# Performance work log

Hardware: AMD Instinct MI355X
Metric: run time of the kernel (lower is better)

## Reference

```python
import jax, jax.numpy as jnp
import numpy as np

B, T, V, D, H, L = 4, 2048, 99, 512, 8, 6
DH = D // H
OFFSET = 28  # size_puzzle_tokens = 1 + 26 + 1
GELU_C = 0.7978845608028654  # sqrt(2/pi)
EPS = 1e-5


def layernorm(x, w):
    m = jnp.mean(x, axis=-1, keepdims=True)
    v = jnp.mean(jnp.square(x - m), axis=-1, keepdims=True)
    return (x - m) / jnp.sqrt(v + EPS) * w


def new_gelu(x):
    return 0.5 * x * (1.0 + jnp.tanh(GELU_C * (x + 0.044715 * x ** 3)))


def setup_inputs() -> dict:
    key = jax.random.key(0)
    ks = jax.random.split(key, 12)
    s = 0.02
    return {
        'idx': jax.random.randint(ks[0], (B, T), 0, V),
        'targets': jax.random.randint(ks[1], (B, T), 0, V),
        'wte': jax.random.normal(ks[2], (V, D), jnp.float32) * s,   # tied with lm_head
        'wpe': jax.random.normal(ks[3], (T, D), jnp.float32) * s,
        'ln1_w': jnp.ones((L, D), jnp.float32),
        'attn_w': jax.random.normal(ks[4], (L, 3 * D, D), jnp.float32) * s,
        'proj_w': jax.random.normal(ks[5], (L, D, D), jnp.float32) * (s / np.sqrt(2 * L)),
        'ln2_w': jnp.ones((L, D), jnp.float32),
        'fc_w': jax.random.normal(ks[6], (L, 4 * D, D), jnp.float32) * s,
        'fc_proj_w': jax.random.normal(ks[7], (L, D, 4 * D), jnp.float32) * (s / np.sqrt(2 * L)),
        'lnf_w': jnp.ones((D,), jnp.float32),
    }


def _forward(idx, targets, wte, wpe, ln1_w, attn_w, proj_w, ln2_w, fc_w, fc_proj_w, lnf_w):
    t = idx.shape[1]
    x = wte[idx] + wpe[:t][None]  # [B,T,D]
    # mask: tril(ones(T+28, T)) narrowed from row 28 -> query i attends keys j <= i+28
    q_ids = jnp.arange(t)
    mask = (q_ids[None, :] <= q_ids[:, None] + OFFSET)  # [T,T]
    scale = 1.0 / np.sqrt(DH)

    def block(x, p):
        w1, wa, wp, w2, wf, wfp = p
        h = layernorm(x, w1)
        qkv = jnp.einsum('btc,oc->bto', h, wa)  # [B,T,3D]
        q, k, v = jnp.split(qkv, 3, axis=-1)
        q = q.reshape(B, t, H, DH)
        k = k.reshape(B, t, H, DH)
        v = v.reshape(B, t, H, DH)
        att = jnp.einsum('bqhd,bkhd->bhqk', q, k) * scale
        att = jnp.where(mask[None, None], att, -jnp.inf)
        att = jax.nn.softmax(att, axis=-1)
        y = jnp.einsum('bhqk,bkhd->bqhd', att, v).reshape(B, t, D)
        y = jnp.einsum('btc,oc->bto', y, wp)
        x = x + y
        h2 = layernorm(x, w2)
        m = new_gelu(jnp.einsum('btc,fc->btf', h2, wf))
        x = x + jnp.einsum('btf,cf->btc', m, wfp)
        return x, None

    x, _ = jax.lax.scan(block, x, (ln1_w, attn_w, proj_w, ln2_w, fc_w, fc_proj_w))
    x = layernorm(x, lnf_w)
    logits = jnp.einsum('btd,vd->btv', x, wte)

    # weighted cross entropy, ignore_index=-1
    ce_w = jnp.zeros((V,), jnp.float32).at[78:96].set(1.0).at[96].set(0.1)
    y = targets.reshape(-1)
    valid = (y != -1)
    yc = jnp.where(valid, y, 0)
    logp = jax.nn.log_softmax(logits.reshape(-1, V), axis=-1)
    nll = -jnp.take_along_axis(logp, yc[:, None], axis=1)[:, 0]
    wi = ce_w[yc] * valid.astype(jnp.float32)
    loss = jnp.sum(wi * nll) / jnp.sum(wi)
    return logits, loss


def reference(idx, targets, wte, wpe, ln1_w, attn_w, proj_w, ln2_w, fc_w, fc_proj_w, lnf_w):
    return _forward(idx, targets, wte, wpe, ln1_w, attn_w, proj_w, ln2_w, fc_w, fc_proj_w, lnf_w)
```

## Files before the change

### kernel.cpp

```cpp
#include <hip/hip_runtime.h>
#include <hip/hip_bf16.h>
#include <math.h>

#define BB 4
#define TT 2048
#define VV 99
#define DD 512
#define HH 8
#define LL 6
#define DHH 64
#define OFFS 28
#define ROWS (BB*TT)

typedef __hip_bfloat16 bf16;
typedef __attribute__((ext_vector_type(8))) short bf16x8;
typedef __attribute__((ext_vector_type(4))) short s16x4;
typedef __attribute__((ext_vector_type(4))) float f32x4;

__device__ __forceinline__ float b2f(bf16 x){ return __bfloat162float(x); }

__device__ __forceinline__ void async_copy16(const void* g, void* l){
    __builtin_amdgcn_global_load_lds(
        (const __attribute__((address_space(1))) unsigned int*)g,
        (__attribute__((address_space(3))) unsigned int*)l, 16, 0, 0);
}

__device__ __forceinline__ unsigned lds_off(const void* p){
    return (unsigned)(size_t)(const __attribute__((address_space(3))) char*)p;
}

#define TRD(dst, a, lit) asm volatile("ds_read_b64_tr_b16 %0, %1 offset:" lit \
                                      : "=v"(dst) : "v"(a) : "memory")
#define CAT8(lo, hi) ((bf16x8)__builtin_shufflevector((lo), (hi), 0,1,2,3,4,5,6,7))

__device__ __forceinline__ unsigned pk2(float a, float b){
    return ((unsigned)(unsigned short)__bfloat16_as_short(__float2bfloat16(a)))
         | ((unsigned)(unsigned short)__bfloat16_as_short(__float2bfloat16(b)) << 16);
}

__device__ __forceinline__ void xcd_swz(int gx, int gy, int &bx, int &by){
    int nwg = gx * gy;
    int orig = by * gx + bx;
    int q = nwg >> 3;
    int nid = (orig & 7) * q + (orig >> 3);
    bx = nid % gx;
    by = nid / gx;
}

__device__ __forceinline__ float wget(const void* w, int mode, size_t i){
    return mode ? b2f(((const bf16*)w)[i]) : ((const float*)w)[i];
}

__global__ void init_kernel(const unsigned int* __restrict__ ln1_bits, float* __restrict__ acc,
                            int* __restrict__ flag){
    acc[0] = 0.f; acc[1] = 0.f;
    flag[0] = (ln1_bits[0] == 0x3F800000u) ? 0 : 1;
}

__global__ __launch_bounds__(256) void wconv_kernel(const void* __restrict__ src,
                                                    bf16* __restrict__ dst, int n,
                                                    const int* __restrict__ flag){
    int mode = flag[0];
    size_t i0 = ((size_t)blockIdx.x*256 + threadIdx.x)*8;
    if (i0 >= (size_t)n) return;
    if (mode == 0){
        const float4* sp = (const float4*)((const float*)src + i0);
        float4 a = sp[0], b = sp[1];
        float f[8] = {a.x,a.y,a.z,a.w, b.x,b.y,b.z,b.w};
        union { short s[8]; uint4 u; } cv;
        #pragma unroll
        for (int k=0;k<8;++k) cv.s[k] = __bfloat16_as_short(__float2bfloat16(f[k]));
        *(uint4*)(dst + i0) = cv.u;
    } else {
        *(uint4*)(dst + i0) = *(const uint4*)((const bf16*)src + i0);
    }
}

__global__ void embed_kernel(const int* __restrict__ idx, const void* __restrict__ wte,
                             const void* __restrict__ wpe, float* __restrict__ x,
                             const int* __restrict__ flag){
    int mode = flag[0];
    int row = blockIdx.x;
    int t = row % TT;
    int tok = idx[row];
    int i = threadIdx.x;
    #pragma unroll
    for (int j = 0; j < 2; ++j){
        int d = i + j*256;
        x[(size_t)row*DD + d] = wget(wte, mode, (size_t)tok*DD + d)
                              + wget(wpe, mode, (size_t)t*DD + d);
    }
}

__global__ void ln_kernel(const float* __restrict__ x, const void* __restrict__ w,
                          size_t woff, bf16* __restrict__ out, const int* __restrict__ flag){
    int mode = flag[0];
    int row = blockIdx.x;
    int lane = threadIdx.x;
    const float* xr = x + (size_t)row*DD;
    float v[8];
    float s = 0.f;
    #pragma unroll
    for (int j=0;j<8;++j){ v[j] = xr[lane + j*64]; s += v[j]; }
    #pragma unroll
    for (int o=32;o;o>>=1) s += __shfl_xor(s,o);
    float mean = s * (1.0f/DD);
    float vs = 0.f;
    #pragma unroll
    for (int j=0;j<8;++j){ float d = v[j]-mean; vs += d*d; }
    #pragma unroll
    for (int o=32;o;o>>=1) vs += __shfl_xor(vs,o);
    float rstd = rsqrtf(vs*(1.0f/DD) + 1e-5f);
    #pragma unroll
    for (int j=0;j<8;++j){
        int d = lane + j*64;
        out[(size_t)row*DD + d] = __float2bfloat16((v[j]-mean)*rstd*wget(w,mode,woff+d));
    }
}

template<int EPI>
__global__ __launch_bounds__(256) void gemm_mfma(const bf16* __restrict__ A,
        const bf16* __restrict__ W, float* __restrict__ C, bf16* __restrict__ Cb,
        int M, int N, int K){
    __shared__ short As[128*32];
    __shared__ short Ws[128*32];
    int tid = threadIdx.x;
    int bx = blockIdx.x, by = blockIdx.y;
    xcd_swz((int)gridDim.x, (int)gridDim.y, bx, by);
    int m0 = by * 128;
    int n0 = bx * 128;
    int lane = tid & 63, wave = tid >> 6;
    int wm = (wave & 1) * 64, wn = (wave >> 1) * 64;
    int quad = lane >> 4, l16 = lane & 15;

    f32x4 acc[4][4] = {};

    int srow = wave*16 + (lane >> 2);
    int scol = (lane & 3) * 8;
    const bf16* ga = A + (size_t)(m0 + srow)*K + scol;
    const bf16* gw = W + (size_t)(n0 + srow)*K + scol;
    short* laA0 = &As[(wave*16)*32];
    short* laA1 = &As[(64 + wave*16)*32];
    short* laW0 = &Ws[(wave*16)*32];
    short* laW1 = &Ws[(64 + wave*16)*32];

    for (int k0 = 0; k0 < K; k0 += 32){
        __syncthreads();
        async_copy16(ga + k0,                 laA0);
        async_copy16(ga + (size_t)64*K + k0,  laA1);
        async_copy16(gw + k0,                 laW0);
        async_copy16(gw + (size_t)64*K + k0,  laW1);
        __syncthreads();

        bf16x8 af[4], bfr[4];
        #pragma unroll
        for (int mi=0;mi<4;++mi)
            af[mi] = *(const bf16x8*)&As[(wm + mi*16 + l16)*32 + quad*8];
        #pragma unroll
        for (int ni=0;ni<4;++ni)
            bfr[ni] = *(const bf16x8*)&Ws[(wn + ni*16 + l16)*32 + quad*8];
        #pragma unroll
        for (int mi=0;mi<4;++mi)
            #pragma unroll
            for (int ni=0;ni<4;++ni)
                acc[mi][ni] = __builtin_amdgcn_mfma_f32_16x16x32_bf16(af[mi], bfr[ni], acc[mi][ni], 0, 0, 0);
    }

    #pragma unroll
    for (int mi=0;mi<4;++mi){
        #pragma unroll
        for (int ni=0;ni<4;++ni){
            int mg = m0 + wm + mi*16 + quad*4;
            int ng = n0 + wn + ni*16 + l16;
            #pragma unroll
            for (int reg=0;reg<4;++reg){
                float val = acc[mi][ni][reg];
                size_t off = (size_t)(mg+reg)*N + ng;
                if (EPI==0){
                    Cb[off] = __float2bfloat16(val);
                } else {
                    float xx = val;
                    float u = 0.7978845608028654f*(xx + 0.044715f*xx*xx*xx);
                    Cb[off] = __float2bfloat16(0.5f*xx*(1.0f+tanhf(u)));
                }
            }
        }
    }
}

__global__ __launch_bounds__(256) void gemm_mfma64(const bf16* __restrict__ A,
        const bf16* __restrict__ W, float* __restrict__ C, int M, int N, int K){
    __shared__ short As[64*32];
    __shared__ short Ws[128*32];
    int tid = threadIdx.x;
    int bx = blockIdx.x, by = blockIdx.y;
    xcd_swz((int)gridDim.x, (int)gridDim.y, bx, by);
    int m0 = by * 64;
    int n0 = bx * 128;
    int lane = tid & 63, wave = tid >> 6;
    int wm = (wave & 1) * 32, wn = (wave >> 1) * 64;
    int quad = lane >> 4, l16 = lane & 15;

    f32x4 acc[2][4] = {};

    int srow = wave*16 + (lane >> 2);
    int scol = (lane & 3) * 8;
    const bf16* ga = A + (size_t)(m0 + srow)*K + scol;
    const bf16* gw = W + (size_t)(n0 + srow)*K + scol;
    short* laA0 = &As[(wave*16)*32];
    short* laW0 = &Ws[(wave*16)*32];
    short* laW1 = &Ws[(64 + wave*16)*32];

    for (int k0 = 0; k0 < K; k0 += 32){
        __syncthreads();
        async_copy16(ga + k0,                 laA0);
        async_copy16(gw + k0,                 laW0);
        async_copy16(gw + (size_t)64*K + k0,  laW1);
        __syncthreads();

        bf16x8 af[2], bfr[4];
        #pragma unroll
        for (int mi=0;mi<2;++mi)
            af[mi] = *(const bf16x8*)&As[(wm + mi*16 + l16)*32 + quad*8];
        #pragma unroll
        for (int ni=0;ni<4;++ni)
            bfr[ni] = *(const bf16x8*)&Ws[(wn + ni*16 + l16)*32 + quad*8];
        #pragma unroll
        for (int mi=0;mi<2;++mi)
            #pragma unroll
            for (int ni=0;ni<4;++ni)
                acc[mi][ni] = __builtin_amdgcn_mfma_f32_16x16x32_bf16(af[mi], bfr[ni], acc[mi][ni], 0, 0, 0);
    }

    #pragma unroll
    for (int mi=0;mi<2;++mi){
        #pragma unroll
        for (int ni=0;ni<4;++ni){
            int mg = m0 + wm + mi*16 + quad*4;
            int ng = n0 + wn + ni*16 + l16;
            #pragma unroll
            for (int reg=0;reg<4;++reg){
                C[(size_t)(mg+reg)*N + ng] += acc[mi][ni][reg];
            }
        }
    }
}

__global__ __launch_bounds__(256) void gemm_nt3(const bf16* __restrict__ A,
        const void* __restrict__ W, size_t woff, float* __restrict__ C,
        int M, int N, int K, const int* __restrict__ flag){
    int mode = flag[0];
    __shared__ float As[16][64];
    __shared__ float Wt[16][64];
    int m0 = blockIdx.y * 64;
    int n0 = blockIdx.x * 64;
    int t = threadIdx.x;
    int tx = t & 15, ty = t >> 4;
    float acc[4][4] = {};
    int am = t >> 2;
    int ak = (t & 3) * 4;

    for (int k0 = 0; k0 < K; k0 += 16){
        {
            const __hip_bfloat162* ap = (const __hip_bfloat162*)(A + (size_t)(m0+am)*K + k0 + ak);
            __hip_bfloat162 p0 = ap[0], p1 = ap[1];
            float2 f0 = __bfloat1622float2(p0), f1 = __bfloat1622float2(p1);
            As[ak+0][am]=f0.x; As[ak+1][am]=f0.y; As[ak+2][am]=f1.x; As[ak+3][am]=f1.y;
        }
        int wn = n0 + am;
        if (wn < N){
            size_t off = woff + (size_t)wn*K + k0 + ak;
            if (mode == 0){
                float4 wv = *(const float4*)((const float*)W + off);
                Wt[ak+0][am]=wv.x; Wt[ak+1][am]=wv.y; Wt[ak+2][am]=wv.z; Wt[ak+3][am]=wv.w;
            } else {
                const __hip_bfloat162* wp = (const __hip_bfloat162*)((const bf16*)W + off);
                __hip_bfloat162 p0 = wp[0], p1 = wp[1];
                float2 f0 = __bfloat1622float2(p0), f1 = __bfloat1622float2(p1);
                Wt[ak+0][am]=f0.x; Wt[ak+1][am]=f0.y; Wt[ak+2][am]=f1.x; Wt[ak+3][am]=f1.y;
            }
        } else {
            Wt[ak+0][am]=0.f; Wt[ak+1][am]=0.f; Wt[ak+2][am]=0.f; Wt[ak+3][am]=0.f;
        }
        __syncthreads();
        #pragma unroll
        for (int kk=0;kk<16;++kk){
            float a[4], b[4];
            #pragma unroll
            for (int i=0;i<4;++i) a[i]=As[kk][ty*4+i];
            #pragma unroll
            for (int j=0;j<4;++j) b[j]=Wt[kk][tx*4+j];
            #pragma unroll
            for (int i=0;i<4;++i)
                #pragma unroll
                for (int j=0;j<4;++j)
                    acc[i][j] += a[i]*b[j];
        }
        __syncthreads();
    }

    #pragma unroll
    for (int i=0;i<4;++i){
        int m = m0 + ty*4 + i;
        #pragma unroll
        for (int j=0;j<4;++j){
            int n = n0 + tx*4 + j;
            if (n >= N) continue;
            C[(size_t)m*N+n] = acc[i][j];
        }
    }
}

__global__ __launch_bounds__(256) void attn_mfma11(const bf16* __restrict__ qkv,
                                                   bf16* __restrict__ y){
    __shared__ __align__(16) short Ks[4][4096];
    __shared__ __align__(16) short Vs[4][4096];
    __shared__ __align__(16) short P2[4][1024];

    int tid = threadIdx.x;
    int lane = tid & 63, wave = tid >> 6;
    int quad = lane >> 4, l16 = lane & 15;

    int bi = blockIdx.x;
    int qt = 31 - (bi >> 5);
    int bh = bi & 31;
    int h = bh & 7;
    int b = bh >> 3;
    int q0 = qt * 64;
    size_t base = (size_t)b * TT * 1536;

    const bf16* qrow = qkv + base + (size_t)(q0 + wave*16 + l16)*1536 + h*64;
    bf16x8 aq0 = *(const bf16x8*)(qrow + quad*8);
    bf16x8 aq1 = *(const bf16x8*)(qrow + 32 + quad*8);

    int kj  = wave*16 + (lane>>3);
    int kgo = ((lane&7) ^ ((lane>>3)&7)) << 3;
    int vj  = ((lane>>3)&3)*8 + ((lane>>5)&1)*4 + ((lane>>1)&3);
    int vdo = wave*16 + ((lane&1)<<3);
    const bf16* ks0 = qkv + base + DD   + h*64 + (size_t)kj*1536 + kgo;
    const bf16* vs0 = qkv + base + 2*DD + h*64 + (size_t)vj*1536 + vdo;
    short* kd = &Ks[0][0] + wave*1024;
    short* vd = &Vs[0][0] + wave*1024;

#define STAGE(bb, j0s) { \
    const bf16* kk_ = ks0 + (size_t)(j0s)*1536; \
    const bf16* vv_ = vs0 + (size_t)(j0s)*1536; \
    short* kdd_ = kd + (bb)*4096; \
    short* vdd_ = vd + (bb)*4096; \
    async_copy16(kk_,                    kdd_); \
    async_copy16(kk_ + (size_t)8*1536,   kdd_ + 512); \
    async_copy16(vv_,                    vdd_); \
    async_copy16(vv_ + (size_t)32*1536,  vdd_ + 512); }

    f32x4 O[4] = {};
    float mr1 = -1e30f;
    float lr1 = 0.f;

    int jbmax = qt + 1; if (jbmax > 31) jbmax = 31;
    int NT = jbmax + 1;

    STAGE(0, 0);
    if (NT > 1) STAGE(1, 64);
    __syncthreads();

    unsigned l8 = (unsigned)(lane << 3);
    unsigned vbase = lds_off(&Vs[0][0]) + l8;
    char* pw = (char*)&P2[wave][0];
    int swz = (l16 & 7) << 4;
    int qg_row = q0 + wave*16 + l16;
    int sb = (quad<<4) | (quad<<2);

#define ATTN_BODY(tt) { \
    int t_ = (tt); \
    int j0 = t_ * 64; \
    const short* kb = &Ks[0][0] + (t_&3)*4096; \
    f32x4 s4[4]; \
    _Pragma("unroll") \
    for (int ni=0; ni<4; ++ni){ \
        int R = ni*16 + l16; \
        int ro = R*64; \
        int sw = R & 7; \
        bf16x8 bk0 = *(const bf16x8*)&kb[ro + ((quad       ^ sw)<<3)]; \
        bf16x8 bk1 = *(const bf16x8*)&kb[ro + (((quad + 4) ^ sw)<<3)]; \
        f32x4 z = {}; \
        z = __builtin_amdgcn_mfma_f32_16x16x32_bf16(bk0, aq0, z, 0, 0, 0); \
        z = __builtin_amdgcn_mfma_f32_16x16x32_bf16(bk1, aq1, z, 0, 0, 0); \
        s4[ni] = z; \
    } \
    float sc[4][4]; \
    bool bd = (j0 + 63 > q0 + OFFS); \
    _Pragma("unroll") \
    for (int ni=0; ni<4; ++ni){ \
        _Pragma("unroll") \
        for (int reg=0; reg<4; ++reg){ \
            float v = s4[ni][reg] * 0.125f; \
            if (bd){ \
                int jg = j0 + ni*16 + quad*4 + reg; \
                if (jg > qg_row + OFFS) v = -1e30f; \
            } \
            sc[ni][reg] = v; \
        } \
    } \
    float mn[4]; \
    _Pragma("unroll") \
    for (int ni=0; ni<4; ++ni) \
        mn[ni] = fmaxf(fmaxf(sc[ni][0], sc[ni][1]), fmaxf(sc[ni][2], sc[ni][3])); \
    float m16 = fmaxf(fmaxf(mn[0], mn[1]), fmaxf(mn[2], mn[3])); \
    m16 = fmaxf(m16, __shfl_xor(m16, 16)); \
    m16 = fmaxf(m16, __shfl_xor(m16, 32)); \
    float nm; \
    float alpha1 = 1.0f; \
    if (__all(m16 <= mr1 + 8.0f)){ \
        nm = mr1;             \
    } else { \
        nm = fmaxf(mr1, m16); \
        alpha1 = __expf(mr1 - nm); \
        mr1 = nm; \
        float al0 = __shfl(alpha1, sb); \
        float al1 = __shfl(alpha1, sb+1); \
        float al2 = __shfl(alpha1, sb+2); \
        float al3 = __shfl(alpha1, sb+3); \
        _Pragma("unroll") \
        for (int dt=0; dt<4; ++dt){ \
            O[dt][0] *= al0; O[dt][1] *= al1; O[dt][2] *= al2; O[dt][3] *= al3; \
        } \
    } \
    float rsn[4]; \
    _Pragma("unroll") \
    for (int ni=0; ni<4; ++ni){ \
        _Pragma("unroll") \
        for (int reg=0; reg<4; ++reg) \
            sc[ni][reg] = __expf(sc[ni][reg] - nm); \
        rsn[ni] = (sc[ni][0] + sc[ni][1]) + (sc[ni][2] + sc[ni][3]); \
    } \
    float rs1 = (rsn[0] + rsn[1]) + (rsn[2] + rsn[3]); \
    rs1 += __shfl_xor(rs1, 16); \
    rs1 += __shfl_xor(rs1, 32); \
    lr1 = lr1*alpha1 + rs1; \
    __builtin_amdgcn_sched_barrier(0); \
    unsigned va = vbase + (unsigned)((t_&3)*8192); \
    s16x4 t000,t001,t010,t011, t100,t101,t110,t111, \
          t200,t201,t210,t211, t300,t301,t310,t311; \
    TRD(t000, va, "0");    TRD(t001, va, "512");  TRD(t010, va, "1024"); TRD(t011, va, "1536"); \
    TRD(t100, va, "2048"); TRD(t101, va, "2560"); TRD(t110, va, "3072"); TRD(t111, va, "3584"); \
    TRD(t200, va, "4096"); TRD(t201, va, "4608"); TRD(t210, va, "5120"); TRD(t211, va, "5632"); \
    TRD(t300, va, "6144"); TRD(t301, va, "6656"); TRD(t310, va, "7168"); TRD(t311, va, "7680"); \
    _Pragma("unroll") \
    for (int ni=0; ni<4; ++ni){ \
        unsigned lo = pk2(sc[ni][0], sc[ni][1]); \
        unsigned hi = pk2(sc[ni][2], sc[ni][3]); \
        *(uint2*)(pw + (((l16<<7) + (ni<<5) + (quad<<3)) ^ swz)) = make_uint2(lo, hi); \
    } \
    bf16x8 ap0 = *(const bf16x8*)(pw + (((l16<<7)      + (quad<<4)) ^ swz)); \
    bf16x8 ap1 = *(const bf16x8*)(pw + (((l16<<7) + 64 + (quad<<4)) ^ swz)); \
    asm volatile("s_waitcnt lgkmcnt(0)" ::: "memory"); \
    __builtin_amdgcn_sched_barrier(0); \
    O[0] = __builtin_amdgcn_mfma_f32_16x16x32_bf16(ap0, CAT8(t000,t001), O[0], 0, 0, 0); \
    O[1] = __builtin_amdgcn_mfma_f32_16x16x32_bf16(ap0, CAT8(t100,t101), O[1], 0, 0, 0); \
    O[2] = __builtin_amdgcn_mfma_f32_16x16x32_bf16(ap0, CAT8(t200,t201), O[2], 0, 0, 0); \
    O[3] = __builtin_amdgcn_mfma_f32_16x16x32_bf16(ap0, CAT8(t300,t301), O[3], 0, 0, 0); \
    O[0] = __builtin_amdgcn_mfma_f32_16x16x32_bf16(ap1, CAT8(t010,t011), O[0], 0, 0, 0); \
    O[1] = __builtin_amdgcn_mfma_f32_16x16x32_bf16(ap1, CAT8(t110,t111), O[1], 0, 0, 0); \
    O[2] = __builtin_amdgcn_mfma_f32_16x16x32_bf16(ap1, CAT8(t210,t211), O[2], 0, 0, 0); \
    O[3] = __builtin_amdgcn_mfma_f32_16x16x32_bf16(ap1, CAT8(t310,t311), O[3], 0, 0, 0); }

    for (int tp = 0; tp < NT; tp += 2){
        if (tp+2 < NT) STAGE((tp+2)&3, (tp+2)*64);
        if (tp+3 < NT) STAGE((tp+3)&3, (tp+3)*64);
        ATTN_BODY(tp);
        if (tp+1 < NT) ATTN_BODY(tp+1);
        __syncthreads();
    }
#undef ATTN_BODY
#undef STAGE

    float invl = 1.0f / lr1;
    float in0 = __shfl(invl, sb);
    float in1 = __shfl(invl, sb+1);
    float in2 = __shfl(invl, sb+2);
    float in3 = __shfl(invl, sb+3);
    float inv[4] = {in0, in1, in2, in3};
    #pragma unroll
    for (int dt=0; dt<4; ++dt){
        #pragma unroll
        for (int reg=0; reg<4; ++reg){
            int qg = q0 + wave*16 + quad*4 + reg;
            y[((size_t)b*TT + qg)*DD + h*64 + dt*16 + l16] =
                __float2bfloat16(O[dt][reg] * inv[reg]);
        }
    }
}

__global__ void loss_kernel(const float* __restrict__ logits, const int* __restrict__ targets,
                            float* __restrict__ acc){
    int row = blockIdx.x;
    int lane = threadIdx.x;
    int yt = targets[row];
    const float* lp = logits + (size_t)row*VV;
    float e0 = (lane < VV)    ? lp[lane]    : -1e30f;
    float e1 = (lane+64 < VV) ? lp[lane+64] : -1e30f;
    float mx = fmaxf(e0,e1);
    #pragma unroll
    for (int o=32;o;o>>=1) mx = fmaxf(mx, __shfl_xor(mx,o));
    float se = 0.f;
    if (lane < VV)    se += __expf(e0-mx);
    if (lane+64 < VV) se += __expf(e1-mx);
    #pragma unroll
    for (int o=32;o;o>>=1) se += __shfl_xor(se,o);
    if (lane == 0 && yt >= 0){
        float wi = (yt>=78 && yt<96) ? 1.0f : (yt==96 ? 0.1f : 0.0f);
        if (wi > 0.f){
            float ly = lp[yt];
            float nll = -(ly - mx - logf(se));
            atomicAdd(&acc[0], wi*nll);
            atomicAdd(&acc[1], wi);
        }
    }
}

__global__ void fin_loss(const float* __restrict__ acc, float* __restrict__ out){
    out[0] = acc[0]/acc[1];
}

extern "C" void kernel_launch(void* const* d_in, const int* in_sizes, int n_in,
                              void* d_out, int out_size, void* d_ws, size_t ws_size,
                              hipStream_t stream){
    const int*  idx     = (const int*) d_in[0];
    const int*  targets = (const int*) d_in[1];
    const void* wte     = d_in[2];
    const void* wpe     = d_in[3];
    const void* ln1_w   = d_in[4];
    const void* attn_w  = d_in[5];
    const void* proj_w  = d_in[6];
    const void* ln2_w   = d_in[7];
    const void* fc_w    = d_in[8];
    const void* fcp_w   = d_in[9];
    const void* lnf_w   = d_in[10];
    float* out = (float*)d_out;

    float* ws   = (float*)d_ws;
    float* ACC  = ws;
    int*   FLAG = (int*)(ws + 4);
    bf16*  Hb   = (bf16*)(ws + 16);
    float* X    = ws + 2097168;
    bf16*  BIG  = (bf16*)(ws + 6291472);
    bf16*  WB   = (bf16*)(ws + 14680080);

    const int ATT_S = 3*DD*DD;
    const int PRJ_S = DD*DD;
    const int FC_S  = 4*DD*DD;
    bf16* WB_att = WB;
    bf16* WB_prj = WB + (size_t)6*ATT_S;
    bf16* WB_fc  = WB_prj + (size_t)6*PRJ_S;
    bf16* WB_fcp = WB_fc  + (size_t)6*FC_S;

    init_kernel<<<1,1,0,stream>>>((const unsigned int*)ln1_w, ACC, FLAG);
    wconv_kernel<<<(6*ATT_S)/2048,256,0,stream>>>(attn_w, WB_att, 6*ATT_S, FLAG);
    wconv_kernel<<<(6*PRJ_S)/2048,256,0,stream>>>(proj_w, WB_prj, 6*PRJ_S, FLAG);
    wconv_kernel<<<(6*FC_S)/2048,256,0,stream>>>(fc_w,  WB_fc,  6*FC_S, FLAG);
    wconv_kernel<<<(6*FC_S)/2048,256,0,stream>>>(fcp_w, WB_fcp, 6*FC_S, FLAG);
    embed_kernel<<<ROWS,256,0,stream>>>(idx, wte, wpe, X, FLAG);
    for (int l=0; l<LL; ++l){
        ln_kernel<<<ROWS,64,0,stream>>>(X, ln1_w, (size_t)l*DD, Hb, FLAG);
        gemm_mfma<0><<<dim3(3*DD/128, ROWS/128),256,0,stream>>>(Hb, WB_att + (size_t)l*ATT_S,
                                                                nullptr, BIG, ROWS, 3*DD, DD);
        attn_mfma11<<<dim3(BB*HH*32),256,0,stream>>>(BIG, Hb);
        gemm_mfma64<<<dim3(DD/128, ROWS/64),256,0,stream>>>(Hb, WB_prj + (size_t)l*PRJ_S,
                                                            X, ROWS, DD, DD);
        ln_kernel<<<ROWS,64,0,stream>>>(X, ln2_w, (size_t)l*DD, Hb, FLAG);
        gemm_mfma<2><<<dim3(4*DD/128, ROWS/128),256,0,stream>>>(Hb, WB_fc + (size_t)l*FC_S,
                                                                nullptr, BIG, ROWS, 4*DD, DD);
        gemm_mfma64<<<dim3(DD/128, ROWS/64),256,0,stream>>>(BIG, WB_fcp + (size_t)l*FC_S,
                                                            X, ROWS, DD, 4*DD);
    }
    ln_kernel<<<ROWS,64,0,stream>>>(X, lnf_w, 0, Hb, FLAG);
    gemm_nt3<<<dim3((VV+63)/64, ROWS/64),256,0,stream>>>(Hb, wte, 0, out, ROWS, VV, DD, FLAG);
    loss_kernel<<<ROWS,64,0,stream>>>(out, targets, ACC);
    fin_loss<<<1,1,0,stream>>>(ACC, out + (size_t)ROWS*VV);
}
```

Baseline: 1.440 ms.

## Double GEMM K-tile to 64 with XOR-swizzled LDS and prescale Q

Both MFMA GEMM kernels now stage 64-wide K slices per iteration instead of 32, which halves the number of barrier pairs per K loop. The LDS layout gets an XOR swizzle on 16-byte chunks to avoid bank conflicts on the fragment reads. The attention kernel folds the 1/sqrt(dh) scale into Q once, since 0.125 is a power of two and exact in bf16, which removes a multiply per score element. The cost is twice the LDS per block, which may lower occupancy.

```diff
diff --git a/kernel.cpp b/kernel.cpp
--- a/kernel.cpp
+++ b/kernel.cpp
@@ -36,6 +36,13 @@
 __device__ __forceinline__ unsigned pk2(float a, float b){
     return ((unsigned)(unsigned short)__bfloat16_as_short(__float2bfloat16(a)))
          | ((unsigned)(unsigned short)__bfloat16_as_short(__float2bfloat16(b)) << 16);
+}
+
+__device__ __forceinline__ short mul125(short s){
+    union { unsigned short u; bf16 b; } cv;
+    cv.u = (unsigned short)s;
+    float f = __bfloat162float(cv.b) * 0.125f;
+    return __bfloat16_as_short(__float2bfloat16(f));
 }
 
 __device__ __forceinline__ void xcd_swz(int gx, int gy, int &bx, int &by){
@@ -122,8 +129,8 @@
 __global__ __launch_bounds__(256) void gemm_mfma(const bf16* __restrict__ A,
         const bf16* __restrict__ W, float* __restrict__ C, bf16* __restrict__ Cb,
         int M, int N, int K){
-    __shared__ short As[128*32];
-    __shared__ short Ws[128*32];
+    __shared__ short As[128*64];
+    __shared__ short Ws[128*64];
     int tid = threadIdx.x;
     int bx = blockIdx.x, by = blockIdx.y;
     xcd_swz((int)gridDim.x, (int)gridDim.y, bx, by);
@@ -135,35 +142,45 @@
 
     f32x4 acc[4][4] = {};
 
-    int srow = wave*16 + (lane >> 2);
-    int scol = (lane & 3) * 8;
+    int srow = wave*32 + (lane >> 3);
+    int scol = ((lane&7) ^ ((lane>>3)&7)) * 8;
     const bf16* ga = A + (size_t)(m0 + srow)*K + scol;
     const bf16* gw = W + (size_t)(n0 + srow)*K + scol;
-    short* laA0 = &As[(wave*16)*32];
-    short* laA1 = &As[(64 + wave*16)*32];
-    short* laW0 = &Ws[(wave*16)*32];
-    short* laW1 = &Ws[(64 + wave*16)*32];
-
-    for (int k0 = 0; k0 < K; k0 += 32){
+    short* dA = &As[(wave*32)*64];
+    short* dW = &Ws[(wave*32)*64];
+
+    for (int k0 = 0; k0 < K; k0 += 64){
         __syncthreads();
-        async_copy16(ga + k0,                 laA0);
-        async_copy16(ga + (size_t)64*K + k0,  laA1);
-        async_copy16(gw + k0,                 laW0);
-        async_copy16(gw + (size_t)64*K + k0,  laW1);
+        async_copy16(ga + k0,                  dA);
+        async_copy16(ga + (size_t)8*K  + k0,   dA + 8*64);
+        async_copy16(ga + (size_t)16*K + k0,   dA + 16*64);
+        async_copy16(ga + (size_t)24*K + k0,   dA + 24*64);
+        async_copy16(gw + k0,                  dW);
+        async_copy16(gw + (size_t)8*K  + k0,   dW + 8*64);
+        async_copy16(gw + (size_t)16*K + k0,   dW + 16*64);
+        async_copy16(gw + (size_t)24*K + k0,   dW + 24*64);
         __syncthreads();
 
-        bf16x8 af[4], bfr[4];
-        #pragma unroll
-        for (int mi=0;mi<4;++mi)
-            af[mi] = *(const bf16x8*)&As[(wm + mi*16 + l16)*32 + quad*8];
-        #pragma unroll
-        for (int ni=0;ni<4;++ni)
-            bfr[ni] = *(const bf16x8*)&Ws[(wn + ni*16 + l16)*32 + quad*8];
-        #pragma unroll
-        for (int mi=0;mi<4;++mi)
-            #pragma unroll
-            for (int ni=0;ni<4;++ni)
-                acc[mi][ni] = __builtin_amdgcn_mfma_f32_16x16x32_bf16(af[mi], bfr[ni], acc[mi][ni], 0, 0, 0);
+        int sw = l16 & 7;
+        #pragma unroll
+        for (int s = 0; s < 2; ++s){
+            bf16x8 af[4], bfr[4];
+            #pragma unroll
+            for (int mi=0;mi<4;++mi){
+                int r = wm + mi*16 + l16;
+                af[mi] = *(const bf16x8*)&As[r*64 + ((((s<<2)|quad) ^ sw)<<3)];
+            }
+            #pragma unroll
+            for (int ni=0;ni<4;++ni){
+                int r = wn + ni*16 + l16;
+                bfr[ni] = *(const bf16x8*)&Ws[r*64 + ((((s<<2)|quad) ^ sw)<<3)];
+            }
+            #pragma unroll
+            for (int mi=0;mi<4;++mi)
+                #pragma unroll
+                for (int ni=0;ni<4;++ni)
+                    acc[mi][ni] = __builtin_amdgcn_mfma_f32_16x16x32_bf16(af[mi], bfr[ni], acc[mi][ni], 0, 0, 0);
+        }
     }
 
     #pragma unroll
@@ -190,8 +207,8 @@
 
 __global__ __launch_bounds__(256) void gemm_mfma64(const bf16* __restrict__ A,
         const bf16* __restrict__ W, float* __restrict__ C, int M, int N, int K){
-    __shared__ short As[64*32];
-    __shared__ short Ws[128*32];
+    __shared__ short As[64*64];
+    __shared__ short Ws[128*64];
     int tid = threadIdx.x;
     int bx = blockIdx.x, by = blockIdx.y;
     xcd_swz((int)gridDim.x, (int)gridDim.y, bx, by);
@@ -203,33 +220,44 @@
 
     f32x4 acc[2][4] = {};
 
-    int srow = wave*16 + (lane >> 2);
-    int scol = (lane & 3) * 8;
-    const bf16* ga = A + (size_t)(m0 + srow)*K + scol;
-    const bf16* gw = W + (size_t)(n0 + srow)*K + scol;
-    short* laA0 = &As[(wave*16)*32];
-    short* laW0 = &Ws[(wave*16)*32];
-    short* laW1 = &Ws[(64 + wave*16)*32];
-
-    for (int k0 = 0; k0 < K; k0 += 32){
+    int scol = ((lane&7) ^ ((lane>>3)&7)) * 8;
+    int srowA = wave*16 + (lane >> 3);
+    int srowW = wave*32 + (lane >> 3);
+    const bf16* ga = A + (size_t)(m0 + srowA)*K + scol;
+    const bf16* gw = W + (size_t)(n0 + srowW)*K + scol;
+    short* dA = &As[(wave*16)*64];
+    short* dW = &Ws[(wave*32)*64];
+
+    for (int k0 = 0; k0 < K; k0 += 64){
         __syncthreads();
-        async_copy16(ga + k0,                 laA0);
-        async_copy16(gw + k0,                 laW0);
-        async_copy16(gw + (size_t)64*K + k0,  laW1);
+        async_copy16(ga + k0,                  dA);
+        async_copy16(ga + (size_t)8*K  + k0,   dA + 8*64);
+        async_copy16(gw + k0,                  dW);
+        async_copy16(gw + (size_t)8*K  + k0,   dW + 8*64);
+        async_copy16(gw + (size_t)16*K + k0,   dW + 16*64);
+        async_copy16(gw + (size_t)24*K + k0,   dW + 24*64);
         __syncthreads();
 
-        bf16x8 af[2], bfr[4];
-        #pragma unroll
-        for (int mi=0;mi<2;++mi)
-            af[mi] = *(const bf16x8*)&As[(wm + mi*16 + l16)*32 + quad*8];
-        #pragma unroll
-        for (int ni=0;ni<4;++ni)
-            bfr[ni] = *(const bf16x8*)&Ws[(wn + ni*16 + l16)*32 + quad*8];
-        #pragma unroll
-        for (int mi=0;mi<2;++mi)
-            #pragma unroll
-            for (int ni=0;ni<4;++ni)
-                acc[mi][ni] = __builtin_amdgcn_mfma_f32_16x16x32_bf16(af[mi], bfr[ni], acc[mi][ni], 0, 0, 0);
+        int sw = l16 & 7;
+        #pragma unroll
+        for (int s = 0; s < 2; ++s){
+            bf16x8 af[2], bfr[4];
+            #pragma unroll
+            for (int mi=0;mi<2;++mi){
+                int r = wm + mi*16 + l16;
+                af[mi] = *(const bf16x8*)&As[r*64 + ((((s<<2)|quad) ^ sw)<<3)];
+            }
+            #pragma unroll
+            for (int ni=0;ni<4;++ni){
+                int r = wn + ni*16 + l16;
+                bfr[ni] = *(const bf16x8*)&Ws[r*64 + ((((s<<2)|quad) ^ sw)<<3)];
+            }
+            #pragma unroll
+            for (int mi=0;mi<2;++mi)
+                #pragma unroll
+                for (int ni=0;ni<4;++ni)
+                    acc[mi][ni] = __builtin_amdgcn_mfma_f32_16x16x32_bf16(af[mi], bfr[ni], acc[mi][ni], 0, 0, 0);
+        }
     }
 
     #pragma unroll
@@ -311,7 +339,7 @@
     }
 }
 
-__global__ __launch_bounds__(256) void attn_mfma11(const bf16* __restrict__ qkv,
+__global__ __launch_bounds__(256) void attn_mfma12(const bf16* __restrict__ qkv,
                                                    bf16* __restrict__ y){
     __shared__ __align__(16) short Ks[4][4096];
     __shared__ __align__(16) short Vs[4][4096];
@@ -332,6 +360,8 @@
     const bf16* qrow = qkv + base + (size_t)(q0 + wave*16 + l16)*1536 + h*64;
     bf16x8 aq0 = *(const bf16x8*)(qrow + quad*8);
     bf16x8 aq1 = *(const bf16x8*)(qrow + 32 + quad*8);
+    #pragma unroll
+    for (int i=0;i<8;++i){ aq0[i] = mul125(aq0[i]); aq1[i] = mul125(aq1[i]); }
 
     int kj  = wave*16 + (lane>>3);
     int kgo = ((lane&7) ^ ((lane>>3)&7)) << 3;
@@ -393,7 +423,7 @@
     for (int ni=0; ni<4; ++ni){ \
         _Pragma("unroll") \
         for (int reg=0; reg<4; ++reg){ \
-            float v = s4[ni][reg] * 0.125f; \
+            float v = s4[ni][reg]; \
             if (bd){ \
                 int jg = j0 + ni*16 + quad*4 + reg; \
                 if (jg > qg_row + OFFS) v = -1e30f; \
@@ -564,7 +594,7 @@
         ln_kernel<<<ROWS,64,0,stream>>>(X, ln1_w, (size_t)l*DD, Hb, FLAG);
         gemm_mfma<0><<<dim3(3*DD/128, ROWS/128),256,0,stream>>>(Hb, WB_att + (size_t)l*ATT_S,
                                                                 nullptr, BIG, ROWS, 3*DD, DD);
-        attn_mfma11<<<dim3(BB*HH*32),256,0,stream>>>(BIG, Hb);
+        attn_mfma12<<<dim3(BB*HH*32),256,0,stream>>>(BIG, Hb);
         gemm_mfma64<<<dim3(DD/128, ROWS/64),256,0,stream>>>(Hb, WB_prj + (size_t)l*PRJ_S,
                                                             X, ROWS, DD, DD);
         ln_kernel<<<ROWS,64,0,stream>>>(X, ln2_w, (size_t)l*DD, Hb, FLAG);
```

Result: no change. 1.419 ms (-1.4%).
